# Kernel tuning notes

Hardware: AMD Instinct MI355X
Metric: run time of the kernel (lower is better)

## Reference

```python
import jax, jax.numpy as jnp
import numpy as np

N_SEG = 64        # number of graphs in batch
NEG_SLOPE = 0.2   # PyG GATConv leaky_relu slope


def seg_softmax(vals, seg, num_segments):
    # vals: [E, H]; softmax over entries sharing the same segment id
    m = jax.ops.segment_max(vals, seg, num_segments=num_segments)
    m = jnp.where(jnp.isfinite(m), m, 0.0)  # guard empty segments
    e = jnp.exp(vals - m[seg])
    s = jax.ops.segment_sum(e, seg, num_segments=num_segments)
    return e / (s[seg] + 1e-16)


def setup_inputs() -> dict:
    key = jax.random.key(0)
    ks = jax.random.split(key, 16)
    N, E, Fin, H, C1, C2 = 50000, 800000, 128, 4, 32, 128
    x = jax.random.normal(ks[0], (N, Fin), jnp.float32)
    edge_index = jax.random.randint(ks[1], (2, E), 0, N)
    batch = jnp.sort(jax.random.randint(ks[2], (N,), 0, N_SEG))
    sc = lambda fan: 1.0 / np.sqrt(fan)
    W_gat = jax.random.normal(ks[3], (Fin, H * C1), jnp.float32) * sc(Fin)
    att_src = jax.random.normal(ks[4], (H, C1), jnp.float32) * sc(C1)
    att_dst = jax.random.normal(ks[5], (H, C1), jnp.float32) * sc(C1)
    b_gat = jnp.zeros((H * C1,), jnp.float32)
    bn1_w = jax.random.uniform(ks[6], (H * C1,), jnp.float32, 0.5, 1.5)
    bn1_b = jax.random.normal(ks[7], (H * C1,), jnp.float32) * 0.1
    W_gcn = jax.random.normal(ks[8], (H * C1, C2), jnp.float32) * sc(H * C1)
    b_gcn = jnp.zeros((C2,), jnp.float32)
    bn2_w = jax.random.uniform(ks[9], (C2,), jnp.float32, 0.5, 1.5)
    bn2_b = jax.random.normal(ks[10], (C2,), jnp.float32) * 0.1
    W_gate = jax.random.normal(ks[11], (C2, 1), jnp.float32) * sc(C2)
    b_gate = jnp.zeros((1,), jnp.float32)
    W_fc = jax.random.normal(ks[12], (C2, 1), jnp.float32) * sc(C2)
    b_fc = jnp.zeros((1,), jnp.float32)
    return dict(x=x, edge_index=edge_index, batch=batch, W_gat=W_gat,
                att_src=att_src, att_dst=att_dst, b_gat=b_gat,
                bn1_w=bn1_w, bn1_b=bn1_b, W_gcn=W_gcn, b_gcn=b_gcn,
                bn2_w=bn2_w, bn2_b=bn2_b, W_gate=W_gate, b_gate=b_gate,
                W_fc=W_fc, b_fc=b_fc)


def reference(x, edge_index, batch, W_gat, att_src, att_dst, b_gat,
              bn1_w, bn1_b, W_gcn, b_gcn, bn2_w, bn2_b,
              W_gate, b_gate, W_fc, b_fc):
    N = x.shape[0]
    H, C1 = att_src.shape
    loops = jnp.arange(N)
    src = jnp.concatenate([edge_index[0], loops])  # message source j
    dst = jnp.concatenate([edge_index[1], loops])  # aggregation target i

    # ---- GATConv (heads=4, concat, add_self_loops) ----
    h = (x @ W_gat).reshape(N, H, C1)                       # [N,H,C1]
    a_src = jnp.einsum('nhc,hc->nh', h, att_src)
    a_dst = jnp.einsum('nhc,hc->nh', h, att_dst)
    e = jax.nn.leaky_relu(a_src[src] + a_dst[dst], NEG_SLOPE)  # [E',H]
    alpha = seg_softmax(e, dst, N)
    msg = h[src] * alpha[..., None]                          # [E',H,C1]
    out1 = jax.ops.segment_sum(msg, dst, num_segments=N).reshape(N, H * C1) + b_gat
    out1 = jax.nn.elu(out1)
    out1 = out1 * bn1_w + bn1_b          # BatchNorm1d (eval: mean 0, var 1)
    # dropout: identity (eval mode)

    # ---- GCNConv (self-loops, symmetric normalization) ----
    deg = jax.ops.segment_sum(jnp.ones_like(dst, dtype=x.dtype), dst, num_segments=N)
    dinv = jax.lax.rsqrt(jnp.maximum(deg, 1.0))
    norm = dinv[src] * dinv[dst]                             # [E']
    h2 = out1 @ W_gcn                                        # [N,C2]
    out2 = jax.ops.segment_sum(h2[src] * norm[:, None], dst, num_segments=N) + b_gcn
    out2 = jax.nn.elu(out2)
    out2 = out2 * bn2_w + bn2_b

    # ---- GlobalAttention pooling ----
    gate = out2 @ W_gate + b_gate                            # [N,1]
    w = seg_softmax(gate, batch, N_SEG)
    graph_rep = jax.ops.segment_sum(w * out2, batch, num_segments=N_SEG)  # [G,C2]

    out = graph_rep @ W_fc + b_fc                            # [G,1]
    return out.squeeze(1)
```

## Files before the change

kernel.cpp:

```cpp
#include <hip/hip_runtime.h>
#include <math.h>


#define NEG_SLOPE 0.2f
#define BKT_BITS 7
#define BKT_SIZE 128
#define CHUNK_A 4096

__device__ __forceinline__ int lower_bound_i(const int* a, int n, int key) {
    int lo = 0, hi = n;
    while (lo < hi) {
        int mid = (lo + hi) >> 1;
        if (a[mid] < key) lo = mid + 1; else hi = mid;
    }
    return lo;
}

__device__ __forceinline__ unsigned pack_bf16(float lo, float hi) {
    unsigned ua = __float_as_uint(lo);
    unsigned ub = __float_as_uint(hi);
    ua = ua + 0x7fffu + ((ua >> 16) & 1u);
    ub = ub + 0x7fffu + ((ub >> 16) & 1u);
    return (ua >> 16) | (ub & 0xffff0000u);
}

__global__ __launch_bounds__(256) void k_gemm(
    const float* __restrict__ A, const float* __restrict__ W,
    unsigned* __restrict__ Cb, int N, int mode,
    const float* __restrict__ pb, const float* __restrict__ pw,
    const float* __restrict__ pb2, const float* __restrict__ dinv,
    const float* __restrict__ atts, const float* __restrict__ attd,
    float* __restrict__ aS, float* __restrict__ aD)
{
    __shared__ float sA[64 * 132];
    const int tid = threadIdx.x;
    const int n0 = blockIdx.x * 64;

    for (int i = tid * 4; i < 64 * 128; i += 1024) {
        int r = i >> 7;
        int k = i & 127;
        int gn = n0 + r;
        float4 v = make_float4(0.f, 0.f, 0.f, 0.f);
        if (gn < N) v = *(const float4*)(A + (size_t)gn * 128 + k);
        if (mode) {
            float4 bv = *(const float4*)(pb + k);
            float4 wv = *(const float4*)(pw + k);
            float4 b2 = *(const float4*)(pb2 + k);
            float t;
            t = v.x + bv.x; t = (t > 0.f) ? t : expm1f(t); v.x = t * wv.x + b2.x;
            t = v.y + bv.y; t = (t > 0.f) ? t : expm1f(t); v.y = t * wv.y + b2.y;
            t = v.z + bv.z; t = (t > 0.f) ? t : expm1f(t); v.z = t * wv.z + b2.z;
            t = v.w + bv.w; t = (t > 0.f) ? t : expm1f(t); v.w = t * wv.w + b2.w;
        }
        *(float4*)(sA + r * 132 + k) = v;
    }
    __syncthreads();

    const int c8 = tid & 15;
    const int cb = c8 * 8;
    const int rg = tid >> 4;
    const int rbase = rg * 4;

    float acc[4][8];
#pragma unroll
    for (int r = 0; r < 4; r++)
#pragma unroll
        for (int c = 0; c < 8; c++) acc[r][c] = 0.f;

    for (int kb = 0; kb < 128; kb += 4) {
        float4 av0 = *(const float4*)(sA + (rbase + 0) * 132 + kb);
        float4 av1 = *(const float4*)(sA + (rbase + 1) * 132 + kb);
        float4 av2 = *(const float4*)(sA + (rbase + 2) * 132 + kb);
        float4 av3 = *(const float4*)(sA + (rbase + 3) * 132 + kb);
        const float* a0f = (const float*)&av0;
        const float* a1f = (const float*)&av1;
        const float* a2f = (const float*)&av2;
        const float* a3f = (const float*)&av3;
#pragma unroll
        for (int j = 0; j < 4; j++) {
            const float* Wrow = W + (size_t)(kb + j) * 128;
            float w[8];
            *(float4*)(w)     = *(const float4*)(Wrow + cb);
            *(float4*)(w + 4) = *(const float4*)(Wrow + cb + 4);
            float aj0 = a0f[j], aj1 = a1f[j], aj2 = a2f[j], aj3 = a3f[j];
#pragma unroll
            for (int c = 0; c < 8; c++) {
                acc[0][c] += aj0 * w[c];
                acc[1][c] += aj1 * w[c];
                acc[2][c] += aj2 * w[c];
                acc[3][c] += aj3 * w[c];
            }
        }
    }

#pragma unroll
    for (int r = 0; r < 4; r++) {
        int gn = n0 + rbase + r;
        if (gn < N) {
            float s = mode ? dinv[gn] : 1.f;
            uint4 pv;
            pv.x = pack_bf16(acc[r][0] * s, acc[r][1] * s);
            pv.y = pack_bf16(acc[r][2] * s, acc[r][3] * s);
            pv.z = pack_bf16(acc[r][4] * s, acc[r][5] * s);
            pv.w = pack_bf16(acc[r][6] * s, acc[r][7] * s);
            *(uint4*)(Cb + (size_t)gn * 64 + (cb >> 1)) = pv;
        }
    }

    if (mode == 0) {
        const int h = c8 >> 2;
        float sat[8], dat[8];
        *(float4*)(sat)     = *(const float4*)(atts + cb);
        *(float4*)(sat + 4) = *(const float4*)(atts + cb + 4);
        *(float4*)(dat)     = *(const float4*)(attd + cb);
        *(float4*)(dat + 4) = *(const float4*)(attd + cb + 4);
#pragma unroll
        for (int r = 0; r < 4; r++) {
            float s = 0.f, d = 0.f;
#pragma unroll
            for (int c = 0; c < 8; c++) { s += acc[r][c] * sat[c]; d += acc[r][c] * dat[c]; }
            s += __shfl_xor(s, 1); s += __shfl_xor(s, 2);
            d += __shfl_xor(d, 1); d += __shfl_xor(d, 2);
            if ((c8 & 3) == 0) {
                int gn = n0 + rbase + r;
                if (gn < N) { aS[(size_t)gn * 4 + h] = s; aD[(size_t)gn * 4 + h] = d; }
            }
        }
    }
}

__global__ __launch_bounds__(256) void k_bhist(const int* __restrict__ dst,
                                               int* __restrict__ bcount,
                                               int E, int NB)
{
    __shared__ int h[512];
    const int tid = threadIdx.x;
    for (int i = tid; i < NB; i += 256) h[i] = 0;
    __syncthreads();
    int base = blockIdx.x * 2048;
#pragma unroll
    for (int k = 0; k < 8; k++) {
        int e = base + k * 256 + tid;
        if (e < E) atomicAdd(&h[dst[e] >> BKT_BITS], 1);
    }
    __syncthreads();
    for (int i = tid; i < NB; i += 256) {
        int c = h[i];
        if (c) atomicAdd(&bcount[i], c);
    }
}

__global__ __launch_bounds__(512) void k_bscan(const int* __restrict__ bcount,
                                               int* __restrict__ bb,
                                               int* __restrict__ bcur, int NB)
{
    __shared__ int sc[512];
    const int tid = threadIdx.x;
    int own = (tid < NB) ? bcount[tid] : 0;
    sc[tid] = own;
    __syncthreads();
    for (int st = 1; st < 512; st <<= 1) {
        int v = 0;
        if (tid >= st) v = sc[tid - st];
        __syncthreads();
        if (tid >= st) sc[tid] += v;
        __syncthreads();
    }
    int excl = sc[tid] - own;
    if (tid < NB) { bb[tid] = excl; bcur[tid] = excl; }
    if (tid == 511) { bb[NB] = sc[511]; bcur[NB] = sc[511]; }
}

__global__ __launch_bounds__(256) void k_binA(const int* __restrict__ ei,
                                              int* __restrict__ bcur,
                                              int2* __restrict__ pairs,
                                              int E, int NB)
{
    __shared__ int h[512];
    __shared__ int base[512];
    const int tid = threadIdx.x;
    for (int i = tid; i < NB + 1; i += 256) h[i] = 0;
    __syncthreads();
    const int c0 = blockIdx.x * CHUNK_A;
    int s[16], d[16], b[16];
#pragma unroll
    for (int k = 0; k < 16; k++) {
        int e = c0 + k * 256 + tid;
        bool v = e < E;
        s[k] = v ? ei[e] : 0;
        d[k] = v ? ei[E + e] : 0;
        b[k] = v ? (d[k] >> BKT_BITS) : NB;
        atomicAdd(&h[b[k]], 1);
    }
    __syncthreads();
    for (int i = tid; i < NB + 1; i += 256) {
        int c = h[i];
        base[i] = c ? atomicAdd(&bcur[i], c) : 0;
        h[i] = 0;
    }
    __syncthreads();
#pragma unroll
    for (int k = 0; k < 16; k++) {
        int r = atomicAdd(&h[b[k]], 1);
        pairs[base[b[k]] + r] = make_int2(s[k], d[k]);
    }
}

__global__ __launch_bounds__(256) void k_binB(const int2* __restrict__ pairs,
                                              const int* __restrict__ bb,
                                              int* __restrict__ csr,
                                              int* __restrict__ offs,
                                              float* __restrict__ dinv,
                                              int N, int NB, int E)
{
    __shared__ int hist[BKT_SIZE], start[BKT_SIZE], cur[BKT_SIZE];
    __shared__ int sc[BKT_SIZE];
    const int tid = threadIdx.x;
    const int b = blockIdx.x;
    const int d0 = b << BKT_BITS;
    const int pbg = bb[b], peg = bb[b + 1];

    if (tid < BKT_SIZE) { hist[tid] = 0; cur[tid] = 0; }
    __syncthreads();
    for (int i = pbg + tid; i < peg; i += 256)
        atomicAdd(&hist[pairs[i].y - d0], 1);
    __syncthreads();
    int own = (tid < BKT_SIZE) ? hist[tid] : 0;
    if (tid < BKT_SIZE) sc[tid] = own;
    __syncthreads();
    for (int st = 1; st < BKT_SIZE; st <<= 1) {
        int v = 0;
        bool act = (tid < BKT_SIZE) && (tid >= st);
        if (act) v = sc[tid - st];
        __syncthreads();
        if (act) sc[tid] += v;
        __syncthreads();
    }
    if (tid < BKT_SIZE) {
        int abs0 = pbg + (sc[tid] - own);
        start[tid] = abs0;
        int d = d0 + tid;
        if (d < N) {
            offs[d] = abs0;
            dinv[d] = rsqrtf((float)(own + 1));
        }
    }
    if (tid == 0 && b == NB - 1) offs[N] = E;
    __syncthreads();
    for (int i = pbg + tid; i < peg; i += 256) {
        int2 p = pairs[i];
        int ld = p.y - d0;
        int r = atomicAdd(&cur[ld], 1);
        csr[start[ld] + r] = p.x;
    }
}

__global__ __launch_bounds__(256) void k_gat_aggr(
    const unsigned* __restrict__ hb, const float* __restrict__ aSg,
    const float* __restrict__ aDg, const int* __restrict__ offs,
    const int* __restrict__ csr, float* __restrict__ raw1, int N)
{
    __shared__ __align__(16) float s_u[4][64][4];
    __shared__ int s_s[4][64];

    const int wid = threadIdx.x >> 6;
    const int lane = threadIdx.x & 63;
    const int n = blockIdx.x * 4 + wid;
    if (n >= N) return;

    const int beg = offs[n];
    const int cnt = offs[n + 1] - beg + 1;
    const float4 ad = *(const float4*)(aDg + (size_t)n * 4);
    const int head = lane >> 4;
    const float* pu = &s_u[wid][0][head];
    const int* ps = &s_s[wid][0];

    float t0 = 0.f, t1 = 0.f, t2 = 0.f, t3 = 0.f;
    float accLo = 0.f, accHi = 0.f;

    for (int base = 0; base < cnt; base += 64) {
        int idx = base + lane;
        bool valid = idx < cnt;
        int src = n;
        if (valid && idx > 0) src = csr[beg + idx - 1];
        float u0 = 0.f, u1 = 0.f, u2 = 0.f, u3 = 0.f;
        if (valid) {
            float4 as = *(const float4*)(aSg + (size_t)src * 4);
            float l0 = as.x + ad.x; l0 = (l0 > 0.f) ? l0 : NEG_SLOPE * l0;
            float l1 = as.y + ad.y; l1 = (l1 > 0.f) ? l1 : NEG_SLOPE * l1;
            float l2 = as.z + ad.z; l2 = (l2 > 0.f) ? l2 : NEG_SLOPE * l2;
            float l3 = as.w + ad.w; l3 = (l3 > 0.f) ? l3 : NEG_SLOPE * l3;
            u0 = __expf(l0); u1 = __expf(l1); u2 = __expf(l2); u3 = __expf(l3);
        }
        t0 += u0; t1 += u1; t2 += u2; t3 += u3;
        s_s[wid][lane] = src;
        *(float4*)&s_u[wid][lane][0] = make_float4(u0, u1, u2, u3);

        int cc = min(64, cnt - base);
        int j = 0;
        for (; j + 8 <= cc; j += 8) {
            int sj[8]; float uj[8]; unsigned vv[8];
#pragma unroll
            for (int k = 0; k < 8; k++) sj[k] = ps[j + k];
#pragma unroll
            for (int k = 0; k < 8; k++) uj[k] = pu[(j + k) * 4];
#pragma unroll
            for (int k = 0; k < 8; k++) vv[k] = hb[sj[k] * 64 + lane];
#pragma unroll
            for (int k = 0; k < 8; k++) {
                float lo = __uint_as_float(vv[k] << 16);
                float hi = __uint_as_float(vv[k] & 0xffff0000u);
                accLo += uj[k] * lo;
                accHi += uj[k] * hi;
            }
        }
        for (; j < cc; j++) {
            int sj = ps[j];
            float uj = pu[j * 4];
            unsigned v = hb[sj * 64 + lane];
            accLo += uj * __uint_as_float(v << 16);
            accHi += uj * __uint_as_float(v & 0xffff0000u);
        }
    }
#pragma unroll
    for (int msk = 1; msk < 64; msk <<= 1) {
        t0 += __shfl_xor(t0, msk);
        t1 += __shfl_xor(t1, msk);
        t2 += __shfl_xor(t2, msk);
        t3 += __shfl_xor(t3, msk);
    }
    float s = (head == 0) ? t0 : (head == 1) ? t1 : (head == 2) ? t2 : t3;
    float inv = 1.f / (s + 1e-16f);
    *(float2*)(raw1 + (size_t)n * 128 + 2 * lane) = make_float2(accLo * inv, accHi * inv);
}

__global__ __launch_bounds__(256) void k_gcn_aggr(
    const unsigned* __restrict__ h2b, const int* __restrict__ offs,
    const int* __restrict__ csr, const float* __restrict__ dinv,
    const float* __restrict__ bgcn,
    const float* __restrict__ bn2w, const float* __restrict__ bn2b,
    const float* __restrict__ wgate, const float* __restrict__ bgate,
    const float* __restrict__ wfc,
    float* __restrict__ gate, float* __restrict__ fcdot, int N)
{
    __shared__ int s_s[4][64];

    const int wid = threadIdx.x >> 6;
    const int lane = threadIdx.x & 63;
    const int n = blockIdx.x * 4 + wid;
    if (n >= N) return;

    const int beg = offs[n];
    const int cnt = offs[n + 1] - beg + 1;
    const float dn = dinv[n];
    const int* ps = &s_s[wid][0];

    float accLo = 0.f, accHi = 0.f;
    for (int base = 0; base < cnt; base += 64) {
        int idx = base + lane;
        int src = n;
        if (idx > 0 && idx < cnt) src = csr[beg + idx - 1];
        s_s[wid][lane] = src;

        int cc = min(64, cnt - base);
        int j = 0;
        for (; j + 8 <= cc; j += 8) {
            int sj[8]; unsigned vv[8];
#pragma unroll
            for (int k = 0; k < 8; k++) sj[k] = ps[j + k];
#pragma unroll
            for (int k = 0; k < 8; k++) vv[k] = h2b[sj[k] * 64 + lane];
#pragma unroll
            for (int k = 0; k < 8; k++) {
                accLo += __uint_as_float(vv[k] << 16);
                accHi += __uint_as_float(vv[k] & 0xffff0000u);
            }
        }
        for (; j < cc; j++) {
            unsigned v = h2b[ps[j] * 64 + lane];
            accLo += __uint_as_float(v << 16);
            accHi += __uint_as_float(v & 0xffff0000u);
        }
    }
    const int c0 = 2 * lane;
    float v0 = dn * accLo + bgcn[c0];
    v0 = (v0 > 0.f) ? v0 : expm1f(v0);
    v0 = v0 * bn2w[c0] + bn2b[c0];
    float v1 = dn * accHi + bgcn[c0 + 1];
    v1 = (v1 > 0.f) ? v1 : expm1f(v1);
    v1 = v1 * bn2w[c0 + 1] + bn2b[c0 + 1];

    float g = v0 * wgate[c0] + v1 * wgate[c0 + 1];
    float f = v0 * wfc[c0]   + v1 * wfc[c0 + 1];
#pragma unroll
    for (int msk = 1; msk < 64; msk <<= 1) {
        g += __shfl_xor(g, msk);
        f += __shfl_xor(f, msk);
    }
    if (lane == 0) { gate[n] = g + bgate[0]; fcdot[n] = f; }
}

__global__ __launch_bounds__(256) void k_pool(
    const float* __restrict__ gate, const float* __restrict__ fcdot,
    const int* __restrict__ batch, const float* __restrict__ bfc,
    float* __restrict__ out, int N)
{
    __shared__ float red[256];
    __shared__ int range[2];
    const int g = blockIdx.x;
    const int tid = threadIdx.x;
    if (tid < 2) range[tid] = lower_bound_i(batch, N, g + tid);
    __syncthreads();
    const int lo = range[0], hi = range[1];
    float se = 0.f, sf = 0.f;
    for (int i = lo + tid; i < hi; i += 256) {
        float e = __expf(gate[i]);
        se += e;
        sf += e * fcdot[i];
    }
    red[tid] = se; __syncthreads();
    for (int s = 128; s > 0; s >>= 1) {
        if (tid < s) red[tid] += red[tid + s];
        __syncthreads();
    }
    se = red[0]; __syncthreads();
    red[tid] = sf; __syncthreads();
    for (int s = 128; s > 0; s >>= 1) {
        if (tid < s) red[tid] += red[tid + s];
        __syncthreads();
    }
    sf = red[0];
    if (tid == 0) out[g] = sf / (se + 1e-16f) + bfc[0];
}

extern "C" void kernel_launch(void* const* d_in, const int* in_sizes, int n_in,
                              void* d_out, int out_size, void* d_ws, size_t ws_size,
                              hipStream_t stream) {
    const float* x     = (const float*)d_in[0];
    const int*   ei    = (const int*)d_in[1];
    const int*   batch = (const int*)d_in[2];
    const float* Wgat  = (const float*)d_in[3];
    const float* atts  = (const float*)d_in[4];
    const float* attd  = (const float*)d_in[5];
    const float* bgat  = (const float*)d_in[6];
    const float* bn1w  = (const float*)d_in[7];
    const float* bn1b  = (const float*)d_in[8];
    const float* Wgcn  = (const float*)d_in[9];
    const float* bgcn  = (const float*)d_in[10];
    const float* bn2w  = (const float*)d_in[11];
    const float* bn2b  = (const float*)d_in[12];
    const float* wgate = (const float*)d_in[13];
    const float* bgate = (const float*)d_in[14];
    const float* wfc   = (const float*)d_in[15];
    const float* bfc   = (const float*)d_in[16];
    float* out = (float*)d_out;

    const int N = in_sizes[0] / 128;
    const int E = in_sizes[1] / 2;
    const int NB = (N + BKT_SIZE - 1) / BKT_SIZE;

    unsigned* hb  = (unsigned*)d_ws;
    unsigned* h2b = hb + (size_t)N * 64;
    float* raw1  = (float*)(h2b + (size_t)N * 64);
    int2* pairs  = (int2*)raw1;
    float* aS    = raw1 + (size_t)N * 128;
    float* aD    = aS + (size_t)N * 4;
    float* gate  = aD + (size_t)N * 4;
    float* fcdot = gate + N;
    float* dinv  = fcdot + N;
    int* offs   = (int*)(dinv + N);
    int* csr    = offs + (N + 1);
    int* bcount = csr + E;
    int* bb     = bcount + (NB + 1);
    int* bcur   = bb + (NB + 1);

    hipMemsetAsync(bcount, 0, (size_t)(NB + 1) * sizeof(int), stream);

    const int gemm_blocks = (N + 63) / 64;
    const int aggr_blocks = (N + 3) / 4;

    k_gemm<<<gemm_blocks, 256, 0, stream>>>(x, Wgat, hb, N, 0,
                                            nullptr, nullptr, nullptr, nullptr,
                                            atts, attd, aS, aD);
    k_bhist<<<(E + 2047) / 2048, 256, 0, stream>>>(ei + E, bcount, E, NB);
    k_bscan<<<1, 512, 0, stream>>>(bcount, bb, bcur, NB);
    k_binA<<<(E + CHUNK_A - 1) / CHUNK_A, 256, 0, stream>>>(ei, bcur, pairs, E, NB);
    k_binB<<<NB, 256, 0, stream>>>(pairs, bb, csr, offs, dinv, N, NB, E);
    k_gat_aggr<<<aggr_blocks, 256, 0, stream>>>(hb, aS, aD, offs, csr, raw1, N);
    k_gemm<<<gemm_blocks, 256, 0, stream>>>(raw1, Wgcn, h2b, N, 1,
                                            bgat, bn1w, bn1b, dinv,
                                            nullptr, nullptr, nullptr, nullptr);
    k_gcn_aggr<<<aggr_blocks, 256, 0, stream>>>(h2b, offs, csr, dinv, bgcn,
                                                bn2w, bn2b, wgate, bgate, wfc,
                                                gate, fcdot, N);
    k_pool<<<64, 256, 0, stream>>>(gate, fcdot, batch, bfc, out, N);
}
```

Measured before the change: 312.6 us.

## Replace scalar FP32 GEMMs with bf16 MFMA and fold attention projections into weights

Both dense layers now run on bf16 MFMA 16x16x32 instructions instead of scalar FP32 FMAs. A small prep kernel transposes and converts the weights to bf16 and appends the attention-source and attention-destination projection columns (W·att) as extra output columns, so aS/aD come out of the same MFMA pass. The bf16 packing layout of the hidden features changes to pair columns c and c+64, and the aggregation kernels are adjusted to match. Inputs and folded weights are rounded to bf16, which adds some numerical error.

```diff
diff --git a/kernel.cpp b/kernel.cpp
--- a/kernel.cpp
+++ b/kernel.cpp
@@ -6,6 +6,9 @@
 #define BKT_BITS 7
 #define BKT_SIZE 128
 #define CHUNK_A 4096
+
+typedef __attribute__((ext_vector_type(8))) short short8v;
+typedef __attribute__((ext_vector_type(4))) float floatx4;
 
 __device__ __forceinline__ int lower_bound_i(const int* a, int n, int key) {
     int lo = 0, hi = n;
@@ -24,107 +27,125 @@
     return (ua >> 16) | (ub & 0xffff0000u);
 }
 
-__global__ __launch_bounds__(256) void k_gemm(
-    const float* __restrict__ A, const float* __restrict__ W,
+__device__ __forceinline__ unsigned short bf16_1(float v) {
+    unsigned u = __float_as_uint(v);
+    u = u + 0x7fffu + ((u >> 16) & 1u);
+    return (unsigned short)(u >> 16);
+}
+
+__global__ __launch_bounds__(1024) void k_prep(
+    const float* __restrict__ W1, const float* __restrict__ atts,
+    const float* __restrict__ attd, const float* __restrict__ W2,
+    unsigned short* __restrict__ Wt1, unsigned short* __restrict__ Wt2)
+{
+    if (blockIdx.x == 0) {
+        for (int idx = threadIdx.x; idx < 144 * 128; idx += 1024) {
+            int j = idx >> 7, i = idx & 127;
+            float v;
+            if (j < 128) v = W1[i * 128 + j];
+            else if (j < 132) {
+                int h = j - 128; float s = 0.f;
+                for (int c = 0; c < 32; c++) s += W1[i * 128 + h * 32 + c] * atts[h * 32 + c];
+                v = s;
+            } else if (j < 136) {
+                int h = j - 132; float s = 0.f;
+                for (int c = 0; c < 32; c++) s += W1[i * 128 + h * 32 + c] * attd[h * 32 + c];
+                v = s;
+            } else v = 0.f;
+            Wt1[idx] = bf16_1(v);
+        }
+    } else {
+        for (int idx = threadIdx.x; idx < 144 * 128; idx += 1024) {
+            int j = idx >> 7, i = idx & 127;
+            Wt2[idx] = bf16_1(j < 128 ? W2[i * 128 + j] : 0.f);
+        }
+    }
+}
+
+__global__ __launch_bounds__(256) void k_gemm_mfma(
+    const float* __restrict__ A, const unsigned short* __restrict__ Wt,
     unsigned* __restrict__ Cb, int N, int mode,
     const float* __restrict__ pb, const float* __restrict__ pw,
     const float* __restrict__ pb2, const float* __restrict__ dinv,
-    const float* __restrict__ atts, const float* __restrict__ attd,
     float* __restrict__ aS, float* __restrict__ aD)
 {
-    __shared__ float sA[64 * 132];
+    __shared__ unsigned short sA[64 * 136];
+    __shared__ unsigned short sB[144 * 136];
     const int tid = threadIdx.x;
     const int n0 = blockIdx.x * 64;
 
-    for (int i = tid * 4; i < 64 * 128; i += 1024) {
-        int r = i >> 7;
-        int k = i & 127;
-        int gn = n0 + r;
-        float4 v = make_float4(0.f, 0.f, 0.f, 0.f);
-        if (gn < N) v = *(const float4*)(A + (size_t)gn * 128 + k);
-        if (mode) {
-            float4 bv = *(const float4*)(pb + k);
-            float4 wv = *(const float4*)(pw + k);
-            float4 b2 = *(const float4*)(pb2 + k);
-            float t;
-            t = v.x + bv.x; t = (t > 0.f) ? t : expm1f(t); v.x = t * wv.x + b2.x;
-            t = v.y + bv.y; t = (t > 0.f) ? t : expm1f(t); v.y = t * wv.y + b2.y;
-            t = v.z + bv.z; t = (t > 0.f) ? t : expm1f(t); v.z = t * wv.z + b2.z;
-            t = v.w + bv.w; t = (t > 0.f) ? t : expm1f(t); v.w = t * wv.w + b2.w;
-        }
-        *(float4*)(sA + r * 132 + k) = v;
-    }
-    __syncthreads();
-
-    const int c8 = tid & 15;
-    const int cb = c8 * 8;
-    const int rg = tid >> 4;
-    const int rbase = rg * 4;
-
-    float acc[4][8];
-#pragma unroll
-    for (int r = 0; r < 4; r++)
-#pragma unroll
-        for (int c = 0; c < 8; c++) acc[r][c] = 0.f;
-
-    for (int kb = 0; kb < 128; kb += 4) {
-        float4 av0 = *(const float4*)(sA + (rbase + 0) * 132 + kb);
-        float4 av1 = *(const float4*)(sA + (rbase + 1) * 132 + kb);
-        float4 av2 = *(const float4*)(sA + (rbase + 2) * 132 + kb);
-        float4 av3 = *(const float4*)(sA + (rbase + 3) * 132 + kb);
-        const float* a0f = (const float*)&av0;
-        const float* a1f = (const float*)&av1;
-        const float* a2f = (const float*)&av2;
-        const float* a3f = (const float*)&av3;
-#pragma unroll
-        for (int j = 0; j < 4; j++) {
-            const float* Wrow = W + (size_t)(kb + j) * 128;
-            float w[8];
-            *(float4*)(w)     = *(const float4*)(Wrow + cb);
-            *(float4*)(w + 4) = *(const float4*)(Wrow + cb + 4);
-            float aj0 = a0f[j], aj1 = a1f[j], aj2 = a2f[j], aj3 = a3f[j];
-#pragma unroll
-            for (int c = 0; c < 8; c++) {
-                acc[0][c] += aj0 * w[c];
-                acc[1][c] += aj1 * w[c];
-                acc[2][c] += aj2 * w[c];
-                acc[3][c] += aj3 * w[c];
+    {
+        const uint4* Wg = (const uint4*)Wt;
+#pragma unroll
+        for (int i = 0; i < 9; i++) {
+            int q = tid + 256 * i;
+            uint4 v = Wg[q];
+            int j = q >> 4, seg = q & 15;
+            *(uint4*)(sB + j * 136 + seg * 8) = v;
+        }
+    }
+    {
+#pragma unroll
+        for (int i = 0; i < 8; i++) {
+            int g = tid + 256 * i;
+            int r = g >> 5, w4 = g & 31;
+            int gn = n0 + r;
+            unsigned p0 = 0, p1 = 0;
+            if (gn < N) {
+                float4 v = *(const float4*)(A + (size_t)gn * 128 + w4 * 4);
+                if (mode) {
+                    int k = w4 * 4;
+                    float4 bv = *(const float4*)(pb + k);
+                    float4 wv = *(const float4*)(pw + k);
+                    float4 b2 = *(const float4*)(pb2 + k);
+                    float t;
+                    t = v.x + bv.x; t = (t > 0.f) ? t : expm1f(t); v.x = t * wv.x + b2.x;
+                    t = v.y + bv.y; t = (t > 0.f) ? t : expm1f(t); v.y = t * wv.y + b2.y;
+                    t = v.z + bv.z; t = (t > 0.f) ? t : expm1f(t); v.z = t * wv.z + b2.z;
+                    t = v.w + bv.w; t = (t > 0.f) ? t : expm1f(t); v.w = t * wv.w + b2.w;
+                }
+                p0 = pack_bf16(v.x, v.y);
+                p1 = pack_bf16(v.z, v.w);
             }
+            uint2 pv = make_uint2(p0, p1);
+            *(uint2*)(sA + r * 136 + w4 * 4) = pv;
+        }
+    }
+    __syncthreads();
+
+    const int wid = tid >> 6, lane = tid & 63;
+    const int quad = lane >> 4, l16 = lane & 15;
+
+    floatx4 acc[9];
+#pragma unroll
+    for (int ct = 0; ct < 9; ct++) acc[ct] = (floatx4){0.f, 0.f, 0.f, 0.f};
+
+    const unsigned short* pa = sA + (wid * 16 + l16) * 136 + quad * 8;
+    const unsigned short* pbt = sB + l16 * 136 + quad * 8;
+#pragma unroll
+    for (int ks = 0; ks < 4; ks++) {
+        short8v a = *(const short8v*)(pa + ks * 32);
+#pragma unroll
+        for (int ct = 0; ct < 9; ct++) {
+            short8v b = *(const short8v*)(pbt + ct * (16 * 136) + ks * 32);
+            acc[ct] = __builtin_amdgcn_mfma_f32_16x16x32_bf16(a, b, acc[ct], 0, 0, 0);
         }
     }
 
 #pragma unroll
     for (int r = 0; r < 4; r++) {
-        int gn = n0 + rbase + r;
-        if (gn < N) {
-            float s = mode ? dinv[gn] : 1.f;
-            uint4 pv;
-            pv.x = pack_bf16(acc[r][0] * s, acc[r][1] * s);
-            pv.y = pack_bf16(acc[r][2] * s, acc[r][3] * s);
-            pv.z = pack_bf16(acc[r][4] * s, acc[r][5] * s);
-            pv.w = pack_bf16(acc[r][6] * s, acc[r][7] * s);
-            *(uint4*)(Cb + (size_t)gn * 64 + (cb >> 1)) = pv;
-        }
-    }
-
-    if (mode == 0) {
-        const int h = c8 >> 2;
-        float sat[8], dat[8];
-        *(float4*)(sat)     = *(const float4*)(atts + cb);
-        *(float4*)(sat + 4) = *(const float4*)(atts + cb + 4);
-        *(float4*)(dat)     = *(const float4*)(attd + cb);
-        *(float4*)(dat + 4) = *(const float4*)(attd + cb + 4);
-#pragma unroll
-        for (int r = 0; r < 4; r++) {
-            float s = 0.f, d = 0.f;
-#pragma unroll
-            for (int c = 0; c < 8; c++) { s += acc[r][c] * sat[c]; d += acc[r][c] * dat[c]; }
-            s += __shfl_xor(s, 1); s += __shfl_xor(s, 2);
-            d += __shfl_xor(d, 1); d += __shfl_xor(d, 2);
-            if ((c8 & 3) == 0) {
-                int gn = n0 + rbase + r;
-                if (gn < N) { aS[(size_t)gn * 4 + h] = s; aD[(size_t)gn * 4 + h] = d; }
-            }
+        int n = n0 + wid * 16 + quad * 4 + r;
+        if (n >= N) continue;
+        float s = mode ? dinv[n] : 1.f;
+#pragma unroll
+        for (int ct = 0; ct < 4; ct++) {
+            Cb[(size_t)n * 64 + ct * 16 + l16] =
+                pack_bf16(acc[ct][r] * s, acc[ct + 4][r] * s);
+        }
+        if (mode == 0) {
+            float e = acc[8][r];
+            if (l16 < 4) aS[(size_t)n * 4 + l16] = e;
+            else if (l16 < 8) aD[(size_t)n * 4 + (l16 - 4)] = e;
         }
     }
 }
@@ -271,8 +292,8 @@
     const int beg = offs[n];
     const int cnt = offs[n + 1] - beg + 1;
     const float4 ad = *(const float4*)(aDg + (size_t)n * 4);
-    const int head = lane >> 4;
-    const float* pu = &s_u[wid][0][head];
+    const int hA = lane >> 5;
+    const float* pu = &s_u[wid][0][2 * hA];
     const int* ps = &s_s[wid][0];
 
     float t0 = 0.f, t1 = 0.f, t2 = 0.f, t3 = 0.f;
@@ -294,32 +315,32 @@
         }
         t0 += u0; t1 += u1; t2 += u2; t3 += u3;
         s_s[wid][lane] = src;
-        *(float4*)&s_u[wid][lane][0] = make_float4(u0, u1, u2, u3);
+        *(float4*)&s_u[wid][lane][0] = make_float4(u0, u2, u1, u3);
 
         int cc = min(64, cnt - base);
         int j = 0;
         for (; j + 8 <= cc; j += 8) {
-            int sj[8]; float uj[8]; unsigned vv[8];
+            int sj[8]; float2 uj[8]; unsigned vv[8];
 #pragma unroll
             for (int k = 0; k < 8; k++) sj[k] = ps[j + k];
 #pragma unroll
-            for (int k = 0; k < 8; k++) uj[k] = pu[(j + k) * 4];
+            for (int k = 0; k < 8; k++) uj[k] = *(const float2*)&pu[(j + k) * 4];
 #pragma unroll
             for (int k = 0; k < 8; k++) vv[k] = hb[sj[k] * 64 + lane];
 #pragma unroll
             for (int k = 0; k < 8; k++) {
                 float lo = __uint_as_float(vv[k] << 16);
                 float hi = __uint_as_float(vv[k] & 0xffff0000u);
-                accLo += uj[k] * lo;
-                accHi += uj[k] * hi;
+                accLo += uj[k].x * lo;
+                accHi += uj[k].y * hi;
             }
         }
         for (; j < cc; j++) {
             int sj = ps[j];
-            float uj = pu[j * 4];
+            float2 uv = *(const float2*)&pu[j * 4];
             unsigned v = hb[sj * 64 + lane];
-            accLo += uj * __uint_as_float(v << 16);
-            accHi += uj * __uint_as_float(v & 0xffff0000u);
+            accLo += uv.x * __uint_as_float(v << 16);
+            accHi += uv.y * __uint_as_float(v & 0xffff0000u);
         }
     }
 #pragma unroll
@@ -329,9 +350,10 @@
         t2 += __shfl_xor(t2, msk);
         t3 += __shfl_xor(t3, msk);
     }
-    float s = (head == 0) ? t0 : (head == 1) ? t1 : (head == 2) ? t2 : t3;
-    float inv = 1.f / (s + 1e-16f);
-    *(float2*)(raw1 + (size_t)n * 128 + 2 * lane) = make_float2(accLo * inv, accHi * inv);
+    float sLo = (hA ? t1 : t0) + 1e-16f;
+    float sHi = (hA ? t3 : t2) + 1e-16f;
+    raw1[(size_t)n * 128 + lane]      = accLo / sLo;
+    raw1[(size_t)n * 128 + 64 + lane] = accHi / sHi;
 }
 
 __global__ __launch_bounds__(256) void k_gcn_aggr(
@@ -382,16 +404,15 @@
             accHi += __uint_as_float(v & 0xffff0000u);
         }
     }
-    const int c0 = 2 * lane;
-    float v0 = dn * accLo + bgcn[c0];
+    float v0 = dn * accLo + bgcn[lane];
     v0 = (v0 > 0.f) ? v0 : expm1f(v0);
-    v0 = v0 * bn2w[c0] + bn2b[c0];
-    float v1 = dn * accHi + bgcn[c0 + 1];
+    v0 = v0 * bn2w[lane] + bn2b[lane];
+    float v1 = dn * accHi + bgcn[lane + 64];
     v1 = (v1 > 0.f) ? v1 : expm1f(v1);
-    v1 = v1 * bn2w[c0 + 1] + bn2b[c0 + 1];
-
-    float g = v0 * wgate[c0] + v1 * wgate[c0 + 1];
-    float f = v0 * wfc[c0]   + v1 * wfc[c0 + 1];
+    v1 = v1 * bn2w[lane + 64] + bn2b[lane + 64];
+
+    float g = v0 * wgate[lane] + v1 * wgate[lane + 64];
+    float f = v0 * wfc[lane]   + v1 * wfc[lane + 64];
 #pragma unroll
     for (int msk = 1; msk < 64; msk <<= 1) {
         g += __shfl_xor(g, msk);
@@ -473,23 +494,26 @@
     int* bcount = csr + E;
     int* bb     = bcount + (NB + 1);
     int* bcur   = bb + (NB + 1);
+    unsigned short* Wt1 = (unsigned short*)(bcur + (NB + 1));
+    unsigned short* Wt2 = Wt1 + 144 * 128;
 
     hipMemsetAsync(bcount, 0, (size_t)(NB + 1) * sizeof(int), stream);
 
     const int gemm_blocks = (N + 63) / 64;
     const int aggr_blocks = (N + 3) / 4;
 
-    k_gemm<<<gemm_blocks, 256, 0, stream>>>(x, Wgat, hb, N, 0,
-                                            nullptr, nullptr, nullptr, nullptr,
-                                            atts, attd, aS, aD);
+    k_prep<<<2, 1024, 0, stream>>>(Wgat, atts, attd, Wgcn, Wt1, Wt2);
     k_bhist<<<(E + 2047) / 2048, 256, 0, stream>>>(ei + E, bcount, E, NB);
+    k_gemm_mfma<<<gemm_blocks, 256, 0, stream>>>(x, Wt1, hb, N, 0,
+                                                 nullptr, nullptr, nullptr,
+                                                 nullptr, aS, aD);
     k_bscan<<<1, 512, 0, stream>>>(bcount, bb, bcur, NB);
     k_binA<<<(E + CHUNK_A - 1) / CHUNK_A, 256, 0, stream>>>(ei, bcur, pairs, E, NB);
     k_binB<<<NB, 256, 0, stream>>>(pairs, bb, csr, offs, dinv, N, NB, E);
     k_gat_aggr<<<aggr_blocks, 256, 0, stream>>>(hb, aS, aD, offs, csr, raw1, N);
-    k_gemm<<<gemm_blocks, 256, 0, stream>>>(raw1, Wgcn, h2b, N, 1,
-                                            bgat, bn1w, bn1b, dinv,
-                                            nullptr, nullptr, nullptr, nullptr);
+    k_gemm_mfma<<<gemm_blocks, 256, 0, stream>>>(raw1, Wt2, h2b, N, 1,
+                                                 bgat, bn1w, bn1b, dinv,
+                                                 nullptr, nullptr);
     k_gcn_aggr<<<aggr_blocks, 256, 0, stream>>>(h2b, offs, csr, dinv, bgcn,
                                                 bn2w, bn2b, wgate, bgate, wfc,
                                                 gate, fcdot, N);
```

After: 276.7 us. 1.13x faster.
